# Optimization experiments

Measured on AMD Instinct MI355X. Metric: run time of the kernel, lower is better.

## Reference

```python
import jax, jax.numpy as jnp
import numpy as np

NEG_SLOPE = 0.2  # GATConv attention leaky_relu slope (init arg)
POST_SLOPE = 0.2  # leaky_relu after LayerNorm in outer forward
N_LAYERS = 3


def _leaky(x, slope):
    return jnp.where(x >= 0, x, slope * x)


def _layer_norm(x, g, b):
    mu = jnp.mean(x, axis=-1, keepdims=True)
    var = jnp.var(x, axis=-1, keepdims=True)
    return (x - mu) * jax.lax.rsqrt(var + 1e-5) * g + b


def _gat_conv(h, W, al, ar, bias, src, dst, apply_act):
    # DGL GATConv (eval mode, dropout = identity)
    N = h.shape[0]
    H, D = al.shape
    feat = (h @ W).reshape(N, H, D)                      # [N,H,D]
    el = jnp.einsum('nhd,hd->nh', feat, al)              # [N,H]
    er = jnp.einsum('nhd,hd->nh', feat, ar)              # [N,H]
    e = _leaky(el[src] + er[dst], NEG_SLOPE)             # [E,H] edge logits
    # segment (per-destination) softmax, numerically stable
    m = jax.ops.segment_max(e, dst, num_segments=N)      # [N,H]
    ex = jnp.exp(e - m[dst])                             # [E,H]
    s = jax.ops.segment_sum(ex, dst, num_segments=N)     # [N,H]
    alpha = ex / s[dst]                                  # [E,H]
    msg = alpha[:, :, None] * feat[src]                  # [E,H,D]
    rst = jax.ops.segment_sum(msg, dst, num_segments=N)  # [N,H,D]
    rst = rst + bias.reshape(1, H, D)
    if apply_act:
        rst = jax.nn.elu(rst)
    return rst


def setup_inputs() -> dict:
    key = jax.random.key(0)
    ks = jax.random.split(key, 12)
    N, E, IN, D, H, C = 100000, 1600000, 256, 64, 4, 40
    HID = H * D  # 256
    sc = 0.05
    return {
        'x': jax.random.normal(ks[0], (N, IN), jnp.float32),
        'W_h': jax.random.normal(ks[1], (3, IN, HID), jnp.float32) * sc,
        'attn_l_h': jax.random.normal(ks[2], (3, H, D), jnp.float32) * sc,
        'attn_r_h': jax.random.normal(ks[3], (3, H, D), jnp.float32) * sc,
        'bias_h': jnp.zeros((3, HID), jnp.float32),
        'ln_g': jnp.ones((3, HID), jnp.float32),
        'ln_b': jnp.zeros((3, HID), jnp.float32),
        'W_o': jax.random.normal(ks[4], (HID, C), jnp.float32) * sc,
        'attn_l_o': jax.random.normal(ks[5], (1, C), jnp.float32) * sc,
        'attn_r_o': jax.random.normal(ks[6], (1, C), jnp.float32) * sc,
        'bias_o': jnp.zeros((C,), jnp.float32),
        'edge_src': jax.random.randint(ks[7], (E,), 0, N, jnp.int32),
        'edge_dst': jax.random.randint(ks[8], (E,), 0, N, jnp.int32),
    }


def reference(x, W_h, attn_l_h, attn_r_h, bias_h, ln_g, ln_b,
              W_o, attn_l_o, attn_r_o, bias_o, edge_src, edge_dst):
    h = x
    for l in range(N_LAYERS):
        hn = _gat_conv(h, W_h[l], attn_l_h[l], attn_r_h[l], bias_h[l],
                       edge_src, edge_dst, True)
        hn = hn.reshape(hn.shape[0], -1)          # flatten heads -> [N, H*D]
        hn = _layer_norm(hn, ln_g[l], ln_b[l])
        hn = _leaky(hn, POST_SLOPE)
        h = hn + h if h.shape == hn.shape else hn  # residual when shapes match
    logits = _gat_conv(h, W_o, attn_l_o, attn_r_o, bias_o,
                       edge_src, edge_dst, False).sum(axis=1)  # sum over heads
    return logits
```

## Files before the change

kernel.cpp:

```cpp
#include <hip/hip_runtime.h>
#include <math.h>


#define NEG_SLOPE 0.2f

typedef __attribute__((ext_vector_type(8))) short bf16x8;
typedef __attribute__((ext_vector_type(4))) float floatx4;

__device__ __forceinline__ float leaky(float x) { return x >= 0.f ? x : NEG_SLOPE * x; }

__device__ __forceinline__ unsigned short f2bf(float f) {
    unsigned u = __builtin_bit_cast(unsigned, f);
    u += 0x7fffu + ((u >> 16) & 1u);
    return (unsigned short)(u >> 16);
}
__device__ __forceinline__ float bf2f(unsigned short h) {
    unsigned u = ((unsigned)h) << 16;
    return __builtin_bit_cast(float, u);
}

__global__ void zero_i32(int* __restrict__ p, int n) {
    int i = blockIdx.x * blockDim.x + threadIdx.x;
    if (i < n) p[i] = 0;
}

__global__ void hist_kernel(const int* __restrict__ dst, int* __restrict__ counts, int E) {
    int e = blockIdx.x * blockDim.x + threadIdx.x;
    if (e < E) atomicAdd(&counts[dst[e]], 1);
}

__global__ __launch_bounds__(256) void scan1(const int* __restrict__ counts,
                                             int* __restrict__ local,
                                             int* __restrict__ bsum, int N) {
    __shared__ int s[256];
    const int t = threadIdx.x;
    const int base = blockIdx.x * 1024 + t * 4;
    int c0 = 0, c1 = 0, c2 = 0, c3 = 0;
    if (base + 3 < N) {
        int4 v = *(const int4*)(counts + base);
        c0 = v.x; c1 = v.y; c2 = v.z; c3 = v.w;
    } else {
        if (base + 0 < N) c0 = counts[base + 0];
        if (base + 1 < N) c1 = counts[base + 1];
        if (base + 2 < N) c2 = counts[base + 2];
    }
    int tsum = c0 + c1 + c2 + c3;
    s[t] = tsum;
    __syncthreads();
    for (int off = 1; off < 256; off <<= 1) {
        int v = (t >= off) ? s[t - off] : 0;
        __syncthreads();
        s[t] += v;
        __syncthreads();
    }
    int excl = s[t] - tsum;
    if (t == 255) bsum[blockIdx.x] = s[255];
    if (base + 0 < N) local[base + 0] = excl;
    if (base + 1 < N) local[base + 1] = excl + c0;
    if (base + 2 < N) local[base + 2] = excl + c0 + c1;
    if (base + 3 < N) local[base + 3] = excl + c0 + c1 + c2;
}

__global__ void scan2(int* __restrict__ bsum, int nb) {
    __shared__ int s[128];
    const int t = threadIdx.x;
    int v = (t < nb) ? bsum[t] : 0;
    s[t] = v;
    __syncthreads();
    for (int off = 1; off < 128; off <<= 1) {
        int u = (t >= off) ? s[t - off] : 0;
        __syncthreads();
        s[t] += u;
        __syncthreads();
    }
    if (t < nb) bsum[t] = s[t] - v;
}

__global__ __launch_bounds__(256) void scan3(const int* __restrict__ local,
                                             const int* __restrict__ bsum,
                                             int* __restrict__ start,
                                             int* __restrict__ cursor, int N) {
    int i = blockIdx.x * 256 + threadIdx.x;
    if (i < N) {
        int v = local[i] + bsum[i >> 10];
        start[i] = v;
        cursor[i] = v;
    }
}

__global__ void scatter_kernel(const int* __restrict__ src, const int* __restrict__ dst,
                               int* __restrict__ cursor, int* __restrict__ col, int E) {
    int e = blockIdx.x * blockDim.x + threadIdx.x;
    if (e < E) {
        int p = atomicAdd(&cursor[dst[e]], 1);
        col[p] = src[e];
    }
}

__global__ void convert_bf(const float* __restrict__ src, unsigned short* __restrict__ dst,
                           int n4) {
    int i = blockIdx.x * blockDim.x + threadIdx.x;
    if (i < n4) {
        float4 v = *(const float4*)(src + (size_t)i * 4);
        ushort4 s;
        s.x = f2bf(v.x); s.y = f2bf(v.y); s.z = f2bf(v.z); s.w = f2bf(v.w);
        *(ushort4*)(dst + (size_t)i * 4) = s;
    }
}

__global__ void transpose_w(const float* __restrict__ W, unsigned short* __restrict__ Wt) {
    int idx = blockIdx.x * 256 + threadIdx.x;
    int l = idx >> 16, r = idx & 65535;
    int k = r >> 8, n = r & 255;
    Wt[l * 65536 + n * 256 + k] = f2bf(W[l * 65536 + k * 256 + n]);
}

__global__ void transpose_wo(const float* __restrict__ W, unsigned short* __restrict__ Wt) {
    int idx = blockIdx.x * 256 + threadIdx.x;
    int n = idx >> 8, k = idx & 255;
    Wt[n * 256 + k] = (n < 40) ? f2bf(W[k * 40 + n]) : (unsigned short)0;
}

#define BPAD 264
#define ALD 40
__global__ __launch_bounds__(512, 2) void gemm_bf16_fused(
    const unsigned short* __restrict__ A, const unsigned short* __restrict__ Wt,
    const float* __restrict__ al, const float* __restrict__ ar,
    unsigned short* __restrict__ Cb, float* __restrict__ el, float* __restrict__ er, int M) {
    __shared__ unsigned short Bs[256 * BPAD];
    __shared__ unsigned short As[2][128 * ALD];
    const int tid = threadIdx.x;
    const int lane = tid & 63, wid = tid >> 6;
    const int wm = (wid >> 2) * 64;
    const int wn = (wid & 3) * 64;
    const int q = lane >> 4, m = lane & 15;

#pragma unroll
    for (int i = 0; i < 16; ++i) {
        int flat = tid + 512 * i;
        int row = flat >> 5, col8 = (flat & 31) * 8;
        *(bf16x8*)&Bs[row * BPAD + col8] = *(const bf16x8*)(Wt + row * 256 + col8);
    }
    __syncthreads();

    const int rA = tid >> 2, k8 = (tid & 3) * 8;
    const int head = wid & 3;
    const float* alh = al + head * 64;
    const float* arh = ar + head * 64;
    const int c = lane & 15;
    float a0 = alh[c], a1 = alh[16 + c], a2 = alh[32 + c], a3 = alh[48 + c];
    float r0 = arh[c], r1 = arh[16 + c], r2 = arh[32 + c], r3 = arh[48 + c];

    const int ntiles = (M + 127) >> 7;
    for (int t = blockIdx.x; t < ntiles; t += gridDim.x) {
        const int row0 = t << 7;
        int agr = row0 + rA; if (agr >= M) agr = M - 1;
        const unsigned short* arow = A + (size_t)agr * 256 + k8;
        bf16x8 pa = *(const bf16x8*)arow;

        floatx4 acc[4][4] = {};
        int cur = 0;
        for (int kb = 0; kb < 256; kb += 32) {
            *(bf16x8*)&As[cur][rA * ALD + k8] = pa;
            __syncthreads();
            if (kb + 32 < 256) pa = *(const bf16x8*)(arow + kb + 32);
            bf16x8 af[4], bfr[4];
#pragma unroll
            for (int i = 0; i < 4; ++i) {
                af[i] = *(const bf16x8*)&As[cur][(wm + i * 16 + m) * ALD + q * 8];
                bfr[i] = *(const bf16x8*)&Bs[(wn + i * 16 + m) * BPAD + kb + q * 8];
            }
#pragma unroll
            for (int i = 0; i < 4; ++i)
#pragma unroll
                for (int j = 0; j < 4; ++j)
                    acc[i][j] = __builtin_amdgcn_mfma_f32_16x16x32_bf16(af[i], bfr[j], acc[i][j], 0, 0, 0);
            cur ^= 1;
        }

#pragma unroll
        for (int i = 0; i < 4; ++i)
#pragma unroll
            for (int j = 0; j < 4; ++j)
#pragma unroll
                for (int r = 0; r < 4; ++r) {
                    int grow = row0 + wm + i * 16 + q * 4 + r;
                    int gcol = wn + j * 16 + c;
                    if (grow < M) Cb[(size_t)grow * 256 + gcol] = f2bf(acc[i][j][r]);
                }

#pragma unroll
        for (int i = 0; i < 4; ++i)
#pragma unroll
            for (int r = 0; r < 4; ++r) {
                float pel = acc[i][0][r] * a0 + acc[i][1][r] * a1 + acc[i][2][r] * a2 + acc[i][3][r] * a3;
                float per = acc[i][0][r] * r0 + acc[i][1][r] * r1 + acc[i][2][r] * r2 + acc[i][3][r] * r3;
#pragma unroll
                for (int off = 8; off >= 1; off >>= 1) {
                    pel += __shfl_xor(pel, off);
                    per += __shfl_xor(per, off);
                }
                if (c == 0) {
                    int grow = row0 + wm + i * 16 + q * 4 + r;
                    if (grow < M) {
                        el[(size_t)grow * 4 + head] = pel;
                        er[(size_t)grow * 4 + head] = per;
                    }
                }
            }
        __syncthreads();
    }
}

#define LDSK 40
#define BSTRIDE 264
__global__ __launch_bounds__(256) void gemm_out_mfma(const unsigned short* __restrict__ h,
                                                     const unsigned short* __restrict__ Wt,
                                                     const float* __restrict__ alo,
                                                     const float* __restrict__ aro,
                                                     unsigned short* __restrict__ feat_o,
                                                     float* __restrict__ elo,
                                                     float* __restrict__ ero, int N) {
    __shared__ unsigned short As[128 * LDSK];
    __shared__ unsigned short Bs[48 * BSTRIDE];
    const int tid = threadIdx.x;
    const int row0 = blockIdx.x * 128;
    const int lane = tid & 63, wid = tid >> 6;

#pragma unroll
    for (int i = 0; i < 6; ++i) {
        int f = tid + 256 * i;
        int n = f >> 5, kk = (f & 31) * 8;
        *(bf16x8*)&Bs[n * BSTRIDE + kk] = *(const bf16x8*)(Wt + n * 256 + kk);
    }
    __syncthreads();

    floatx4 acc[2][3] = {};
    for (int kb = 0; kb < 256; kb += 32) {
#pragma unroll
        for (int i = 0; i < 2; ++i) {
            int idx = tid + 256 * i;
            int r = idx >> 2, k8 = (idx & 3) * 8;
            int gr = row0 + r;
            bf16x8 v = {};
            if (gr < N) v = *(const bf16x8*)(h + (size_t)gr * 256 + kb + k8);
            *(bf16x8*)&As[r * LDSK + k8] = v;
        }
        __syncthreads();
        const int q = lane >> 4, m = lane & 15;
        bf16x8 af[2], bfr[3];
#pragma unroll
        for (int i = 0; i < 2; ++i)
            af[i] = *(const bf16x8*)&As[(wid * 32 + i * 16 + m) * LDSK + q * 8];
#pragma unroll
        for (int j = 0; j < 3; ++j)
            bfr[j] = *(const bf16x8*)&Bs[(j * 16 + m) * BSTRIDE + kb + q * 8];
#pragma unroll
        for (int i = 0; i < 2; ++i)
#pragma unroll
            for (int j = 0; j < 3; ++j)
                acc[i][j] = __builtin_amdgcn_mfma_f32_16x16x32_bf16(af[i], bfr[j], acc[i][j], 0, 0, 0);
        __syncthreads();
    }

    const int q = lane >> 4, c = lane & 15;
#pragma unroll
    for (int i = 0; i < 2; ++i)
#pragma unroll
        for (int j = 0; j < 3; ++j)
#pragma unroll
            for (int r = 0; r < 4; ++r) {
                int grow = row0 + wid * 32 + i * 16 + q * 4 + r;
                int gcol = j * 16 + c;
                if (grow < N && gcol < 40) feat_o[(size_t)grow * 40 + gcol] = f2bf(acc[i][j][r]);
            }

    float aj[3], rj[3];
#pragma unroll
    for (int j = 0; j < 3; ++j) {
        int gcol = j * 16 + c;
        aj[j] = gcol < 40 ? alo[gcol] : 0.f;
        rj[j] = gcol < 40 ? aro[gcol] : 0.f;
    }
#pragma unroll
    for (int i = 0; i < 2; ++i)
#pragma unroll
        for (int r = 0; r < 4; ++r) {
            float pl = acc[i][0][r] * aj[0] + acc[i][1][r] * aj[1] + acc[i][2][r] * aj[2];
            float pr = acc[i][0][r] * rj[0] + acc[i][1][r] * rj[1] + acc[i][2][r] * rj[2];
#pragma unroll
            for (int off = 8; off >= 1; off >>= 1) {
                pl += __shfl_xor(pl, off);
                pr += __shfl_xor(pr, off);
            }
            if (c == 0) {
                int grow = row0 + wid * 32 + i * 16 + q * 4 + r;
                if (grow < N) {
                    elo[grow] = pl;
                    ero[grow] = pr;
                }
            }
        }
}

__global__ __launch_bounds__(256) void aggregate_hidden(
    const unsigned short* __restrict__ feat, const float* __restrict__ el,
    const float* __restrict__ er, const int* __restrict__ start, const int* __restrict__ endp,
    const int* __restrict__ col, const float* __restrict__ bias, const float* __restrict__ lng,
    const float* __restrict__ lnb, const unsigned short* __restrict__ h_in,
    unsigned short* __restrict__ h_out, int node0, int nend) {
    int node = node0 + blockIdx.x * 4 + (threadIdx.x >> 6);
    int lane = threadIdx.x & 63;
    if (node >= nend) return;
    int begin = __builtin_amdgcn_readfirstlane(start[node]);
    int end = __builtin_amdgcn_readfirstlane(endp[node]);
    const int head = lane >> 4;
    const float erh = er[(size_t)node * 4 + head];

    const int ch = lane * 4;
    const unsigned short* fbase = feat + ch;
    const size_t hstr = 256;
    float4 acc = {0.f, 0.f, 0.f, 0.f};
    float ssum = 0.f;
    int e = begin;
    for (; e + 7 < end; e += 8) {
        int sA = col[e], sB = col[e + 1], sC = col[e + 2], sD = col[e + 3];
        int sE = col[e + 4], sF = col[e + 5], sG = col[e + 6], sH = col[e + 7];
        float eA = el[(size_t)sA * 4 + head];
        float eB = el[(size_t)sB * 4 + head];
        float eC = el[(size_t)sC * 4 + head];
        float eD = el[(size_t)sD * 4 + head];
        float eE = el[(size_t)sE * 4 + head];
        float eF = el[(size_t)sF * 4 + head];
        float eG = el[(size_t)sG * 4 + head];
        float eH = el[(size_t)sH * 4 + head];
        ushort4 uA = *(const ushort4*)(fbase + sA * hstr);
        ushort4 uB = *(const ushort4*)(fbase + sB * hstr);
        ushort4 uC = *(const ushort4*)(fbase + sC * hstr);
        ushort4 uD = *(const ushort4*)(fbase + sD * hstr);
        ushort4 uE = *(const ushort4*)(fbase + sE * hstr);
        ushort4 uF = *(const ushort4*)(fbase + sF * hstr);
        ushort4 uG = *(const ushort4*)(fbase + sG * hstr);
        ushort4 uH = *(const ushort4*)(fbase + sH * hstr);
        float wA = __expf(leaky(eA + erh));
        float wB = __expf(leaky(eB + erh));
        float wC = __expf(leaky(eC + erh));
        float wD = __expf(leaky(eD + erh));
        float wE = __expf(leaky(eE + erh));
        float wF = __expf(leaky(eF + erh));
        float wG = __expf(leaky(eG + erh));
        float wH = __expf(leaky(eH + erh));
        ssum += wA + wB + wC + wD + wE + wF + wG + wH;
        acc.x = fmaf(wA, bf2f(uA.x), acc.x); acc.y = fmaf(wA, bf2f(uA.y), acc.y);
        acc.z = fmaf(wA, bf2f(uA.z), acc.z); acc.w = fmaf(wA, bf2f(uA.w), acc.w);
        acc.x = fmaf(wB, bf2f(uB.x), acc.x); acc.y = fmaf(wB, bf2f(uB.y), acc.y);
        acc.z = fmaf(wB, bf2f(uB.z), acc.z); acc.w = fmaf(wB, bf2f(uB.w), acc.w);
        acc.x = fmaf(wC, bf2f(uC.x), acc.x); acc.y = fmaf(wC, bf2f(uC.y), acc.y);
        acc.z = fmaf(wC, bf2f(uC.z), acc.z); acc.w = fmaf(wC, bf2f(uC.w), acc.w);
        acc.x = fmaf(wD, bf2f(uD.x), acc.x); acc.y = fmaf(wD, bf2f(uD.y), acc.y);
        acc.z = fmaf(wD, bf2f(uD.z), acc.z); acc.w = fmaf(wD, bf2f(uD.w), acc.w);
        acc.x = fmaf(wE, bf2f(uE.x), acc.x); acc.y = fmaf(wE, bf2f(uE.y), acc.y);
        acc.z = fmaf(wE, bf2f(uE.z), acc.z); acc.w = fmaf(wE, bf2f(uE.w), acc.w);
        acc.x = fmaf(wF, bf2f(uF.x), acc.x); acc.y = fmaf(wF, bf2f(uF.y), acc.y);
        acc.z = fmaf(wF, bf2f(uF.z), acc.z); acc.w = fmaf(wF, bf2f(uF.w), acc.w);
        acc.x = fmaf(wG, bf2f(uG.x), acc.x); acc.y = fmaf(wG, bf2f(uG.y), acc.y);
        acc.z = fmaf(wG, bf2f(uG.z), acc.z); acc.w = fmaf(wG, bf2f(uG.w), acc.w);
        acc.x = fmaf(wH, bf2f(uH.x), acc.x); acc.y = fmaf(wH, bf2f(uH.y), acc.y);
        acc.z = fmaf(wH, bf2f(uH.z), acc.z); acc.w = fmaf(wH, bf2f(uH.w), acc.w);
    }
    for (; e < end; ++e) {
        int sA = col[e];
        float wA = __expf(leaky(el[(size_t)sA * 4 + head] + erh));
        ushort4 uA = *(const ushort4*)(fbase + sA * hstr);
        ssum += wA;
        acc.x = fmaf(wA, bf2f(uA.x), acc.x); acc.y = fmaf(wA, bf2f(uA.y), acc.y);
        acc.z = fmaf(wA, bf2f(uA.z), acc.z); acc.w = fmaf(wA, bf2f(uA.w), acc.w);
    }
    float inv = ssum > 0.f ? 1.f / ssum : 0.f;
    acc.x *= inv; acc.y *= inv; acc.z *= inv; acc.w *= inv;

    float4 bb = *(const float4*)(bias + ch);
    float x0 = acc.x + bb.x, x1 = acc.y + bb.y, x2 = acc.z + bb.z, x3 = acc.w + bb.w;
    x0 = x0 > 0.f ? x0 : expm1f(x0);
    x1 = x1 > 0.f ? x1 : expm1f(x1);
    x2 = x2 > 0.f ? x2 : expm1f(x2);
    x3 = x3 > 0.f ? x3 : expm1f(x3);
    float lsum = x0 + x1 + x2 + x3;
    float lsq = x0 * x0 + x1 * x1 + x2 * x2 + x3 * x3;
#pragma unroll
    for (int off = 32; off >= 1; off >>= 1) {
        lsum += __shfl_xor(lsum, off);
        lsq += __shfl_xor(lsq, off);
    }
    float mu = lsum * (1.f / 256.f);
    float var = lsq * (1.f / 256.f) - mu * mu;
    float rstd = rsqrtf(var + 1e-5f);
    float4 g4 = *(const float4*)(lng + ch);
    float4 b4 = *(const float4*)(lnb + ch);
    ushort4 hi = *(const ushort4*)(h_in + (size_t)node * 256 + ch);
    float y0 = (x0 - mu) * rstd * g4.x + b4.x;
    float y1 = (x1 - mu) * rstd * g4.y + b4.y;
    float y2 = (x2 - mu) * rstd * g4.z + b4.z;
    float y3 = (x3 - mu) * rstd * g4.w + b4.w;
    y0 = (y0 >= 0.f ? y0 : 0.2f * y0) + bf2f(hi.x);
    y1 = (y1 >= 0.f ? y1 : 0.2f * y1) + bf2f(hi.y);
    y2 = (y2 >= 0.f ? y2 : 0.2f * y2) + bf2f(hi.z);
    y3 = (y3 >= 0.f ? y3 : 0.2f * y3) + bf2f(hi.w);
    ushort4 o;
    o.x = f2bf(y0); o.y = f2bf(y1); o.z = f2bf(y2); o.w = f2bf(y3);
    *(ushort4*)(h_out + (size_t)node * 256 + ch) = o;
}

__global__ __launch_bounds__(256) void aggregate_out(const unsigned short* __restrict__ feat_o,
                                                     const float* __restrict__ elo,
                                                     const float* __restrict__ ero,
                                                     const int* __restrict__ start,
                                                     const int* __restrict__ endp,
                                                     const int* __restrict__ col,
                                                     const float* __restrict__ bias_o,
                                                     float* __restrict__ out, int N) {
    int node = blockIdx.x * 4 + (threadIdx.x >> 6);
    int lane = threadIdx.x & 63;
    if (node >= N) return;
    int begin = __builtin_amdgcn_readfirstlane(start[node]);
    int end = __builtin_amdgcn_readfirstlane(endp[node]);
    float ern = ero[node];
    int cc = lane < 40 ? lane : 0;
    float acc = 0.f, ssum = 0.f;
    int e = begin;
    for (; e + 7 < end; e += 8) {
        int sA = col[e], sB = col[e + 1], sC = col[e + 2], sD = col[e + 3];
        int sE = col[e + 4], sF = col[e + 5], sG = col[e + 6], sH = col[e + 7];
        float eA = elo[sA], eB = elo[sB], eC = elo[sC], eD = elo[sD];
        float eE = elo[sE], eF = elo[sF], eG = elo[sG], eH = elo[sH];
        unsigned short fA = feat_o[(size_t)sA * 40 + cc];
        unsigned short fB = feat_o[(size_t)sB * 40 + cc];
        unsigned short fC = feat_o[(size_t)sC * 40 + cc];
        unsigned short fD = feat_o[(size_t)sD * 40 + cc];
        unsigned short fE = feat_o[(size_t)sE * 40 + cc];
        unsigned short fF = feat_o[(size_t)sF * 40 + cc];
        unsigned short fG = feat_o[(size_t)sG * 40 + cc];
        unsigned short fH = feat_o[(size_t)sH * 40 + cc];
        float wA = __expf(leaky(eA + ern));
        float wB = __expf(leaky(eB + ern));
        float wC = __expf(leaky(eC + ern));
        float wD = __expf(leaky(eD + ern));
        float wE = __expf(leaky(eE + ern));
        float wF = __expf(leaky(eF + ern));
        float wG = __expf(leaky(eG + ern));
        float wH = __expf(leaky(eH + ern));
        ssum += wA + wB + wC + wD + wE + wF + wG + wH;
        acc = fmaf(wA, bf2f(fA), acc);
        acc = fmaf(wB, bf2f(fB), acc);
        acc = fmaf(wC, bf2f(fC), acc);
        acc = fmaf(wD, bf2f(fD), acc);
        acc = fmaf(wE, bf2f(fE), acc);
        acc = fmaf(wF, bf2f(fF), acc);
        acc = fmaf(wG, bf2f(fG), acc);
        acc = fmaf(wH, bf2f(fH), acc);
    }
    for (; e < end; ++e) {
        int sA = col[e];
        float wA = __expf(leaky(elo[sA] + ern));
        ssum += wA;
        acc = fmaf(wA, bf2f(feat_o[(size_t)sA * 40 + cc]), acc);
    }
    float inv = ssum > 0.f ? 1.f / ssum : 0.f;
    if (lane < 40) out[(size_t)node * 40 + lane] = acc * inv + bias_o[lane];
}

extern "C" void kernel_launch(void* const* d_in, const int* in_sizes, int n_in,
                              void* d_out, int out_size, void* d_ws, size_t ws_size,
                              hipStream_t stream) {
    const float* x = (const float*)d_in[0];
    const float* W_h = (const float*)d_in[1];
    const float* al_h = (const float*)d_in[2];
    const float* ar_h = (const float*)d_in[3];
    const float* bias_h = (const float*)d_in[4];
    const float* ln_g = (const float*)d_in[5];
    const float* ln_b = (const float*)d_in[6];
    const float* W_o = (const float*)d_in[7];
    const float* al_o = (const float*)d_in[8];
    const float* ar_o = (const float*)d_in[9];
    const float* bias_o = (const float*)d_in[10];
    const int* esrc = (const int*)d_in[11];
    const int* edst = (const int*)d_in[12];
    const int N = in_sizes[0] / 256;
    const int E = in_sizes[11];
    float* out = (float*)d_out;

    char* ws = (char*)d_ws;
    size_t off = 0;
    auto walloc = [&](size_t bytes) -> void* {
        void* p = ws + off;
        off += (bytes + 255) & ~(size_t)255;
        return p;
    };
    unsigned short* x_bf = (unsigned short*)walloc((size_t)N * 256 * 2);
    unsigned short* h_bf = (unsigned short*)walloc((size_t)N * 256 * 2);
    unsigned short* feat_bf = (unsigned short*)walloc((size_t)N * 256 * 2);
    unsigned short* Wt = (unsigned short*)walloc((size_t)3 * 65536 * 2);
    unsigned short* Wt_o = (unsigned short*)walloc((size_t)48 * 256 * 2);
    float* el = (float*)walloc((size_t)N * 4 * 4);
    float* er = (float*)walloc((size_t)N * 4 * 4);
    int* counts = (int*)walloc(((size_t)N + 1) * 4);
    int* start = (int*)walloc((size_t)N * 4);
    int* endp = (int*)walloc((size_t)N * 4);
    int* col = (int*)walloc((size_t)E * 4);
    int* lscan = (int*)walloc((size_t)N * 4);
    int* bsum = (int*)walloc(128 * 4);
    if (off > ws_size) return;

    const int TB = 256;
    const int nbscan = (N + 1023) / 1024;
    convert_bf<<<(N * 64 + TB - 1) / TB, TB, 0, stream>>>(x, x_bf, N * 64);
    transpose_w<<<3 * 65536 / TB, TB, 0, stream>>>(W_h, Wt);
    transpose_wo<<<48, TB, 0, stream>>>(W_o, Wt_o);
    zero_i32<<<(N + TB - 1) / TB, TB, 0, stream>>>(counts, N);
    hist_kernel<<<(E + TB - 1) / TB, TB, 0, stream>>>(edst, counts, E);
    scan1<<<nbscan, TB, 0, stream>>>(counts, lscan, bsum, N);
    scan2<<<1, 128, 0, stream>>>(bsum, nbscan);
    scan3<<<(N + TB - 1) / TB, TB, 0, stream>>>(lscan, bsum, start, endp, N);
    scatter_kernel<<<(E + TB - 1) / TB, TB, 0, stream>>>(esrc, edst, endp, col, E);

    const int N2 = ((N / 2) + 3) & ~3;
    const int nbh1 = (N2 + 3) / 4;
    const int nbh2 = (N - N2 + 3) / 4;
    for (int l = 0; l < 3; ++l) {
        const unsigned short* hin = (l == 0) ? x_bf : h_bf;
        gemm_bf16_fused<<<256, 512, 0, stream>>>(hin, Wt + (size_t)l * 65536,
                                                 al_h + l * 256, ar_h + l * 256,
                                                 feat_bf, el, er, N);
        aggregate_hidden<<<nbh1, 256, 0, stream>>>(feat_bf, el, er, start, endp, col,
                                                   bias_h + l * 256, ln_g + l * 256,
                                                   ln_b + l * 256, hin, h_bf, 0, N2);
        aggregate_hidden<<<nbh2, 256, 0, stream>>>(feat_bf, el, er, start, endp, col,
                                                   bias_h + l * 256, ln_g + l * 256,
                                                   ln_b + l * 256, hin, h_bf, N2, N);
    }
    unsigned short* feat_o = feat_bf;
    float* elo = el;
    float* ero = er;
    gemm_out_mfma<<<(N + 127) / 128, 256, 0, stream>>>(h_bf, Wt_o, al_o, ar_o, feat_o, elo, ero, N);
    aggregate_out<<<(N + 3) / 4, 256, 0, stream>>>(feat_o, elo, ero, start, endp, col, bias_o, out, N);
}
```

Measured before the change: 999.0 us.

## Build CSR via two-level bucket partition with shared-memory atomics

Replaces the global-atomic histogram, three-pass scan and random scatter with a bucketed counting sort. Edges are first partitioned into 128-node buckets using shared-memory histograms, then each bucket builds its CSR segment locally. The aim is to cut global atomic contention and scattered writes during CSR construction, at the cost of an extra E*8-byte pairs buffer and one more pass over the edges. The output aggregation is also split into two launches over node halves, mirroring the hidden layers.

```diff
diff --git a/kernel.cpp b/kernel.cpp
--- a/kernel.cpp
+++ b/kernel.cpp
@@ -24,27 +24,37 @@
     if (i < n) p[i] = 0;
 }
 
-__global__ void hist_kernel(const int* __restrict__ dst, int* __restrict__ counts, int E) {
-    int e = blockIdx.x * blockDim.x + threadIdx.x;
-    if (e < E) atomicAdd(&counts[dst[e]], 1);
-}
-
-__global__ __launch_bounds__(256) void scan1(const int* __restrict__ counts,
-                                             int* __restrict__ local,
-                                             int* __restrict__ bsum, int N) {
+__global__ __launch_bounds__(256) void bucket_count(const int* __restrict__ dst,
+                                                    int* __restrict__ bcnt, int E, int nbkt) {
+    __shared__ int h[1024];
+    for (int i = threadIdx.x; i < nbkt; i += 256) h[i] = 0;
+    __syncthreads();
+    const int base = blockIdx.x * 8192;
+#pragma unroll 4
+    for (int i = 0; i < 32; ++i) {
+        int e = base + threadIdx.x + i * 256;
+        if (e < E) atomicAdd(&h[dst[e] >> 7], 1);
+    }
+    __syncthreads();
+    for (int i = threadIdx.x; i < nbkt; i += 256) {
+        int v = h[i];
+        if (v) atomicAdd(&bcnt[i], v);
+    }
+}
+
+__global__ __launch_bounds__(256) void bucket_scan(const int* __restrict__ bcnt,
+                                                   int* __restrict__ bbase,
+                                                   int* __restrict__ bcursor, int nbkt) {
     __shared__ int s[256];
     const int t = threadIdx.x;
-    const int base = blockIdx.x * 1024 + t * 4;
-    int c0 = 0, c1 = 0, c2 = 0, c3 = 0;
-    if (base + 3 < N) {
-        int4 v = *(const int4*)(counts + base);
-        c0 = v.x; c1 = v.y; c2 = v.z; c3 = v.w;
-    } else {
-        if (base + 0 < N) c0 = counts[base + 0];
-        if (base + 1 < N) c1 = counts[base + 1];
-        if (base + 2 < N) c2 = counts[base + 2];
-    }
-    int tsum = c0 + c1 + c2 + c3;
+    int c[4];
+    int tsum = 0;
+#pragma unroll
+    for (int j = 0; j < 4; ++j) {
+        int i = t * 4 + j;
+        c[j] = (i < nbkt) ? bcnt[i] : 0;
+        tsum += c[j];
+    }
     s[t] = tsum;
     __syncthreads();
     for (int off = 1; off < 256; off <<= 1) {
@@ -54,46 +64,89 @@
         __syncthreads();
     }
     int excl = s[t] - tsum;
-    if (t == 255) bsum[blockIdx.x] = s[255];
-    if (base + 0 < N) local[base + 0] = excl;
-    if (base + 1 < N) local[base + 1] = excl + c0;
-    if (base + 2 < N) local[base + 2] = excl + c0 + c1;
-    if (base + 3 < N) local[base + 3] = excl + c0 + c1 + c2;
-}
-
-__global__ void scan2(int* __restrict__ bsum, int nb) {
+#pragma unroll
+    for (int j = 0; j < 4; ++j) {
+        int i = t * 4 + j;
+        if (i < nbkt) {
+            bbase[i] = excl;
+            bcursor[i] = excl;
+        }
+        excl += c[j];
+    }
+}
+
+__global__ __launch_bounds__(256) void bucket_partition(const int* __restrict__ src,
+                                                        const int* __restrict__ dst,
+                                                        int* __restrict__ bcursor,
+                                                        int2* __restrict__ pairs, int E, int nbkt) {
+    __shared__ int h[1024];
+    __shared__ int basech[1024];
+    for (int i = threadIdx.x; i < nbkt; i += 256) h[i] = 0;
+    __syncthreads();
+    const int base = blockIdx.x * 8192;
+#pragma unroll 4
+    for (int i = 0; i < 32; ++i) {
+        int e = base + threadIdx.x + i * 256;
+        if (e < E) atomicAdd(&h[dst[e] >> 7], 1);
+    }
+    __syncthreads();
+    for (int i = threadIdx.x; i < nbkt; i += 256) {
+        int v = h[i];
+        basech[i] = v ? atomicAdd(&bcursor[i], v) : 0;
+    }
+    __syncthreads();
+    for (int i = threadIdx.x; i < nbkt; i += 256) h[i] = 0;
+    __syncthreads();
+#pragma unroll 4
+    for (int i = 0; i < 32; ++i) {
+        int e = base + threadIdx.x + i * 256;
+        if (e < E) {
+            int d = dst[e], b = d >> 7;
+            int r = atomicAdd(&h[b], 1);
+            pairs[basech[b] + r] = make_int2(src[e], d);
+        }
+    }
+}
+
+__global__ __launch_bounds__(256) void csr_bucket(const int2* __restrict__ pairs,
+                                                  const int* __restrict__ bbase,
+                                                  int* __restrict__ start, int* __restrict__ endp,
+                                                  int* __restrict__ col, int N, int E, int nbkt) {
+    const int b = blockIdx.x;
+    const int node0 = b << 7;
+    int nc = N - node0;
+    if (nc <= 0) return;
+    if (nc > 128) nc = 128;
+    __shared__ int cnt[128];
     __shared__ int s[128];
     const int t = threadIdx.x;
-    int v = (t < nb) ? bsum[t] : 0;
-    s[t] = v;
+    if (t < 128) cnt[t] = 0;
+    __syncthreads();
+    const int ebase = bbase[b];
+    const int eend = (b + 1 < nbkt) ? bbase[b + 1] : E;
+    for (int e = ebase + t; e < eend; e += 256) {
+        atomicAdd(&cnt[pairs[e].y - node0], 1);
+    }
+    __syncthreads();
+    if (t < 128) s[t] = cnt[t];
     __syncthreads();
     for (int off = 1; off < 128; off <<= 1) {
-        int u = (t >= off) ? s[t - off] : 0;
+        int v = 0;
+        if (t < 128 && t >= off) v = s[t - off];
         __syncthreads();
-        s[t] += u;
+        if (t < 128) s[t] += v;
         __syncthreads();
     }
-    if (t < nb) bsum[t] = s[t] - v;
-}
-
-__global__ __launch_bounds__(256) void scan3(const int* __restrict__ local,
-                                             const int* __restrict__ bsum,
-                                             int* __restrict__ start,
-                                             int* __restrict__ cursor, int N) {
-    int i = blockIdx.x * 256 + threadIdx.x;
-    if (i < N) {
-        int v = local[i] + bsum[i >> 10];
-        start[i] = v;
-        cursor[i] = v;
-    }
-}
-
-__global__ void scatter_kernel(const int* __restrict__ src, const int* __restrict__ dst,
-                               int* __restrict__ cursor, int* __restrict__ col, int E) {
-    int e = blockIdx.x * blockDim.x + threadIdx.x;
-    if (e < E) {
-        int p = atomicAdd(&cursor[dst[e]], 1);
-        col[p] = src[e];
+    if (t < nc) {
+        start[node0 + t] = ebase + s[t] - cnt[t];
+        endp[node0 + t] = ebase + s[t];
+    }
+    if (t < 128) cnt[t] = s[t] - cnt[t];
+    __syncthreads();
+    for (int e = ebase + t; e < eend; e += 256) {
+        int2 pr = pairs[e];
+        int r = atomicAdd(&cnt[pr.y - node0], 1);
+        col[ebase + r] = pr.x;
     }
 }
 
@@ -418,10 +471,10 @@
                                                      const int* __restrict__ endp,
                                                      const int* __restrict__ col,
                                                      const float* __restrict__ bias_o,
-                                                     float* __restrict__ out, int N) {
-    int node = blockIdx.x * 4 + (threadIdx.x >> 6);
+                                                     float* __restrict__ out, int node0, int nend) {
+    int node = node0 + blockIdx.x * 4 + (threadIdx.x >> 6);
     int lane = threadIdx.x & 63;
-    if (node >= N) return;
+    if (node >= nend) return;
     int begin = __builtin_amdgcn_readfirstlane(start[node]);
     int end = __builtin_amdgcn_readfirstlane(endp[node]);
     float ern = ero[node];
@@ -503,25 +556,26 @@
     unsigned short* Wt_o = (unsigned short*)walloc((size_t)48 * 256 * 2);
     float* el = (float*)walloc((size_t)N * 4 * 4);
     float* er = (float*)walloc((size_t)N * 4 * 4);
-    int* counts = (int*)walloc(((size_t)N + 1) * 4);
     int* start = (int*)walloc((size_t)N * 4);
     int* endp = (int*)walloc((size_t)N * 4);
     int* col = (int*)walloc((size_t)E * 4);
-    int* lscan = (int*)walloc((size_t)N * 4);
-    int* bsum = (int*)walloc(128 * 4);
+    int* bcnt = (int*)walloc(1024 * 4);
+    int* bbase = (int*)walloc(1024 * 4);
+    int* bcursor = (int*)walloc(1024 * 4);
+    int2* pairs = (int2*)walloc((size_t)E * 8);
     if (off > ws_size) return;
 
     const int TB = 256;
-    const int nbscan = (N + 1023) / 1024;
+    const int nbkt = (N + 127) >> 7;
+    const int nbe = (E + 8191) / 8192;
     convert_bf<<<(N * 64 + TB - 1) / TB, TB, 0, stream>>>(x, x_bf, N * 64);
     transpose_w<<<3 * 65536 / TB, TB, 0, stream>>>(W_h, Wt);
     transpose_wo<<<48, TB, 0, stream>>>(W_o, Wt_o);
-    zero_i32<<<(N + TB - 1) / TB, TB, 0, stream>>>(counts, N);
-    hist_kernel<<<(E + TB - 1) / TB, TB, 0, stream>>>(edst, counts, E);
-    scan1<<<nbscan, TB, 0, stream>>>(counts, lscan, bsum, N);
-    scan2<<<1, 128, 0, stream>>>(bsum, nbscan);
-    scan3<<<(N + TB - 1) / TB, TB, 0, stream>>>(lscan, bsum, start, endp, N);
-    scatter_kernel<<<(E + TB - 1) / TB, TB, 0, stream>>>(esrc, edst, endp, col, E);
+    zero_i32<<<(nbkt + TB - 1) / TB, TB, 0, stream>>>(bcnt, nbkt);
+    bucket_count<<<nbe, TB, 0, stream>>>(edst, bcnt, E, nbkt);
+    bucket_scan<<<1, TB, 0, stream>>>(bcnt, bbase, bcursor, nbkt);
+    bucket_partition<<<nbe, TB, 0, stream>>>(esrc, edst, bcursor, pairs, E, nbkt);
+    csr_bucket<<<nbkt, TB, 0, stream>>>(pairs, bbase, start, endp, col, N, E, nbkt);
 
     const int N2 = ((N / 2) + 3) & ~3;
     const int nbh1 = (N2 + 3) / 4;
@@ -542,5 +596,6 @@
     float* elo = el;
     float* ero = er;
     gemm_out_mfma<<<(N + 127) / 128, 256, 0, stream>>>(h_bf, Wt_o, al_o, ar_o, feat_o, elo, ero, N);
-    aggregate_out<<<(N + 3) / 4, 256, 0, stream>>>(feat_o, elo, ero, start, endp, col, bias_o, out, N);
-}
+    aggregate_out<<<nbh1, 256, 0, stream>>>(feat_o, elo, ero, start, endp, col, bias_o, out, 0, N2);
+    aggregate_out<<<nbh2, 256, 0, stream>>>(feat_o, elo, ero, start, endp, col, bias_o, out, N2, N);
+}
```

Result: faster. 905.6 us (-9.4%).
